# Optimization experiments

Hardware: AMD Instinct MI355X
Metric: run time of the kernel (lower is better)

The kernel has to match this reference:

```python
import jax, jax.numpy as jnp
import numpy as np

N_NODES = 100000
N_EDGES = 1600000
IN_F, HID_F, OUT_F = 128, 128, 128


def setup_inputs() -> dict:
    key = jax.random.key(0)
    k1, k2, k3, k4, k5, k6 = jax.random.split(key, 6)
    x = jax.random.normal(k1, (N_NODES, IN_F), dtype=jnp.float32)
    edge_index = jax.random.randint(k2, (2, N_EDGES), 0, N_NODES, dtype=jnp.int32)
    # nn.Linear params (PyTorch layout: W [out, in], y = x @ W.T + b)
    s1 = 1.0 / np.sqrt(IN_F)
    W1 = jax.random.uniform(k3, (HID_F, IN_F), minval=-s1, maxval=s1, dtype=jnp.float32)
    b1 = jax.random.uniform(k4, (HID_F,), minval=-s1, maxval=s1, dtype=jnp.float32)
    s2 = 1.0 / np.sqrt(HID_F)
    W2 = jax.random.uniform(k5, (OUT_F, HID_F), minval=-s2, maxval=s2, dtype=jnp.float32)
    b2 = jax.random.uniform(k6, (OUT_F,), minval=-s2, maxval=s2, dtype=jnp.float32)
    return {"x": x, "edge_index": edge_index, "W1": W1, "b1": b1, "W2": W2, "b2": b2}


def _spmm_mean(h, row, col, deg_inv):
    # (adj @ h)[i] = sum_{edges e: row[e]==i} h[col[e]], then scale by deg_inv[i]
    agg = jax.ops.segment_sum(h[col], row, num_segments=N_NODES)
    return agg * deg_inv[:, None]


def reference(x, edge_index, W1, b1, W2, b2):
    row, col = edge_index[0], edge_index[1]
    # degree = row-sum of adjacency (duplicates in COO are summed, matching torch)
    deg = jax.ops.segment_sum(jnp.ones((N_EDGES,), dtype=x.dtype), row, num_segments=N_NODES)
    deg_inv = jnp.where(deg > 0, 1.0 / deg, 0.0)
    # dropout in eval mode = identity
    h = x @ W1.T + b1
    h = _spmm_mean(h, row, col, deg_inv)
    h = jax.nn.elu(h)
    h = h @ W2.T + b2
    h = _spmm_mean(h, row, col, deg_inv)
    return h
```

## Files before the change

### kernel.cpp

```cpp
#include <hip/hip_runtime.h>
#include <math.h>

#define N_NODES 100000
#define N_EDGES 1600000
#define F 128
#define NBUCK 196
#define EPB 1024
#define CAP 9216

typedef _Float16 f16x2 __attribute__((ext_vector_type(2)));
typedef _Float16 f16x8 __attribute__((ext_vector_type(8)));
typedef __fp16 fp16x2 __attribute__((ext_vector_type(2)));
typedef float f32x2 __attribute__((ext_vector_type(2)));
typedef float f32x4 __attribute__((ext_vector_type(4)));

__device__ inline uint pkrtz(float a, float b) {
    union { fp16x2 h; uint u; } c;
    c.h = __builtin_amdgcn_cvt_pkrtz(a, b);
    return c.u;
}
__device__ inline f16x2 as2(uint u) {
    union { uint u; f16x2 h; } c; c.u = u; return c.h;
}

__device__ inline int wave_incl_scan(int v, int lane) {
#pragma unroll
    for (int off = 1; off < 64; off <<= 1) {
        int t = __shfl_up(v, off);
        if (lane >= off) v += t;
    }
    return v;
}


__global__ __launch_bounds__(256) void bucketize_kernel(const int* __restrict__ row,
                                                        const int* __restrict__ col,
                                                        int* __restrict__ bucket_cursor,
                                                        int* __restrict__ pairs) {
    __shared__ int stage[EPB];
    __shared__ unsigned char bid[EPB];
    __shared__ int lcnt[NBUCK], lcur[NBUCK], loff[NBUCK], gbase[NBUCK];
    __shared__ int wsum[4];
    const int tid = threadIdx.x;
    const int lane = tid & 63;
    const int wid = tid >> 6;
    const int base = blockIdx.x * EPB;
    const int cnt = min(N_EDGES - base, EPB);

    for (int i = tid; i < NBUCK; i += 256) { lcnt[i] = 0; lcur[i] = 0; }
    __syncthreads();
    for (int i = 0; i < EPB / 256; ++i) {
        int e = base + i * 256 + tid;
        if (e < N_EDGES) atomicAdd(&lcnt[row[e] >> 9], 1);
    }
    __syncthreads();
    {
        int v = (tid < NBUCK) ? lcnt[tid] : 0;
        int inc = wave_incl_scan(v, lane);
        if (lane == 63) wsum[wid] = inc;
        __syncthreads();
        if (tid == 0) {
            int a = 0;
#pragma unroll
            for (int i = 0; i < 4; ++i) { int t = wsum[i]; wsum[i] = a; a += t; }
        }
        __syncthreads();
        if (tid < NBUCK) loff[tid] = inc - v + wsum[wid];
    }
    if (tid < NBUCK) {
        int c = lcnt[tid];
        gbase[tid] = c ? atomicAdd(&bucket_cursor[tid], c) : 0;
    }
    __syncthreads();
    for (int i = 0; i < EPB / 256; ++i) {
        int e = base + i * 256 + tid;
        if (e < N_EDGES) {
            int r = row[e], c = col[e];
            int b = r >> 9;
            int rk = atomicAdd(&lcur[b], 1);
            int q = loff[b] + rk;
            stage[q] = ((r & 511) << 17) | c;
            bid[q] = (unsigned char)b;
        }
    }
    __syncthreads();
    for (int q = tid; q < cnt; q += 256) {
        int b = bid[q];
        int t = gbase[b] + (q - loff[b]);
        if (t < CAP) pairs[b * CAP + t] = stage[q];
    }
}

__global__ __launch_bounds__(1024) void csr_finalize_kernel(const int* __restrict__ pairs,
                                                            const int* __restrict__ bucket_cursor,
                                                            int* __restrict__ csr_col,
                                                            int2* __restrict__ rs,
                                                            float* __restrict__ deg_inv) {
    __shared__ int rcnt[512], rcnt2[512], roff[512];
    __shared__ int colstage[CAP];
    __shared__ int wsum[8];
    const int tid = threadIdx.x;
    const int lane = tid & 63;
    const int wid = tid >> 6;
    const int b = blockIdx.x;
    const int cnt = min(bucket_cursor[b], CAP);
    const int base = b * CAP;
    const int* reg = &pairs[base];

    if (tid < 512) { rcnt[tid] = 0; rcnt2[tid] = 0; }
    __syncthreads();
    for (int q = tid; q < cnt; q += 1024) atomicAdd(&rcnt[reg[q] >> 17], 1);
    __syncthreads();
    int d = 0, inc = 0;
    if (tid < 512) {
        d = rcnt[tid];
        inc = wave_incl_scan(d, lane);
        if (lane == 63) wsum[wid] = inc;
    }
    __syncthreads();
    if (tid == 0) {
        int a = 0;
#pragma unroll
        for (int i = 0; i < 8; ++i) { int t = wsum[i]; wsum[i] = a; a += t; }
    }
    __syncthreads();
    if (tid < 512) {
        const int excl = inc - d + wsum[wid];
        roff[tid] = excl;
        const int grow = (b << 9) + tid;
        if (grow < N_NODES) {
            rs[grow] = make_int2(base + excl, d);
            deg_inv[grow] = d ? 1.0f / (float)d : 0.0f;
        }
    }
    __syncthreads();
    for (int q = tid; q < cnt; q += 1024) {
        int v = reg[q];
        int lr = v >> 17;
        int rk = atomicAdd(&rcnt2[lr], 1);
        colstage[roff[lr] + rk] = v & 0x1FFFF;
    }
    __syncthreads();
    for (int q = tid; q < cnt; q += 1024) csr_col[base + q] = colstage[q];
}


__global__ __launch_bounds__(256) void convert_w_kernel(const float* __restrict__ W1,
                                                        const float* __restrict__ W2,
                                                        uint* __restrict__ W1h,
                                                        uint* __restrict__ W2h) {
    int i = blockIdx.x * 256 + threadIdx.x;
    if (i < F * F / 2) {
        float2 a = *(const float2*)&W1[i * 2];
        float2 b = *(const float2*)&W2[i * 2];
        W1h[i] = pkrtz(a.x, a.y);
        W2h[i] = pkrtz(b.x, b.y);
    }
}

__global__ __launch_bounds__(256) void convert_x_kernel(const float* __restrict__ X,
                                                        uint* __restrict__ Xh) {
    int i = blockIdx.x * 256 + threadIdx.x;
    if (i < N_NODES * F / 8) {
        float4 a = *(const float4*)&X[(size_t)i * 8];
        float4 b = *(const float4*)&X[(size_t)i * 8 + 4];
        uint4 o = {pkrtz(a.x, a.y), pkrtz(a.z, a.w), pkrtz(b.x, b.y), pkrtz(b.z, b.w)};
        *(uint4*)&Xh[(size_t)i * 4] = o;
    }
}


template <bool ELU, bool OUT_F32>
__global__ __launch_bounds__(64, 8) void fused_agg_gemm_kernel(
        const ushort* __restrict__ H,
        const int2* __restrict__ rs,
        const int* __restrict__ csr_col,
        const float* __restrict__ deg_inv,
        const ushort* __restrict__ Wh,
        const float* __restrict__ bias,
        void* __restrict__ out) {
    __shared__ __align__(16) ushort xs[16 * 136];

    const int tid = threadIdx.x;
    const int m0 = blockIdx.x << 4;
    const int qw = tid >> 4;
    const int fo = (tid & 15) << 3;

    for (int rr = 0; rr < 4; ++rr) {
        const int rowi = qw * 4 + rr;
        const int node = m0 + rowi;
        f32x2 a[4];
#pragma unroll
        for (int i = 0; i < 4; ++i) a[i] = (f32x2){0.f, 0.f};
        const int2 sd = rs[node];
        int p = sd.x;
        const int e = sd.x + sd.y;
        const float di = deg_inv[node];
        while (p + 7 < e) {
            int cc[8];
#pragma unroll
            for (int k = 0; k < 8; ++k) cc[k] = __builtin_nontemporal_load(&csr_col[p + k]);
            uint4 vv[8];
#pragma unroll
            for (int k = 0; k < 8; ++k) vv[k] = *(const uint4*)&H[(size_t)cc[k] * F + fo];
#pragma unroll
            for (int k = 0; k < 8; k += 4) {
                f16x2 h0 = (as2(vv[k].x) + as2(vv[k + 1].x)) + (as2(vv[k + 2].x) + as2(vv[k + 3].x));
                f16x2 h1 = (as2(vv[k].y) + as2(vv[k + 1].y)) + (as2(vv[k + 2].y) + as2(vv[k + 3].y));
                f16x2 h2 = (as2(vv[k].z) + as2(vv[k + 1].z)) + (as2(vv[k + 2].z) + as2(vv[k + 3].z));
                f16x2 h3 = (as2(vv[k].w) + as2(vv[k + 1].w)) + (as2(vv[k + 2].w) + as2(vv[k + 3].w));
                a[0] += (f32x2){(float)h0.x, (float)h0.y};
                a[1] += (f32x2){(float)h1.x, (float)h1.y};
                a[2] += (f32x2){(float)h2.x, (float)h2.y};
                a[3] += (f32x2){(float)h3.x, (float)h3.y};
            }
            p += 8;
        }
        if (p + 3 < e) {
            int c0 = csr_col[p], c1 = csr_col[p + 1], c2 = csr_col[p + 2], c3 = csr_col[p + 3];
            uint4 v0 = *(const uint4*)&H[(size_t)c0 * F + fo];
            uint4 v1 = *(const uint4*)&H[(size_t)c1 * F + fo];
            uint4 v2 = *(const uint4*)&H[(size_t)c2 * F + fo];
            uint4 v3 = *(const uint4*)&H[(size_t)c3 * F + fo];
            f16x2 h0 = (as2(v0.x) + as2(v1.x)) + (as2(v2.x) + as2(v3.x));
            f16x2 h1 = (as2(v0.y) + as2(v1.y)) + (as2(v2.y) + as2(v3.y));
            f16x2 h2 = (as2(v0.z) + as2(v1.z)) + (as2(v2.z) + as2(v3.z));
            f16x2 h3 = (as2(v0.w) + as2(v1.w)) + (as2(v2.w) + as2(v3.w));
            a[0] += (f32x2){(float)h0.x, (float)h0.y};
            a[1] += (f32x2){(float)h1.x, (float)h1.y};
            a[2] += (f32x2){(float)h2.x, (float)h2.y};
            a[3] += (f32x2){(float)h3.x, (float)h3.y};
            p += 4;
        }
        if (p + 1 < e) {
            int c0 = csr_col[p], c1 = csr_col[p + 1];
            uint4 v0 = *(const uint4*)&H[(size_t)c0 * F + fo];
            uint4 v1 = *(const uint4*)&H[(size_t)c1 * F + fo];
            f16x2 h0 = as2(v0.x) + as2(v1.x);
            f16x2 h1 = as2(v0.y) + as2(v1.y);
            f16x2 h2 = as2(v0.z) + as2(v1.z);
            f16x2 h3 = as2(v0.w) + as2(v1.w);
            a[0] += (f32x2){(float)h0.x, (float)h0.y};
            a[1] += (f32x2){(float)h1.x, (float)h1.y};
            a[2] += (f32x2){(float)h2.x, (float)h2.y};
            a[3] += (f32x2){(float)h3.x, (float)h3.y};
            p += 2;
        }
        if (p < e) {
            int c = csr_col[p];
            uint4 v = *(const uint4*)&H[(size_t)c * F + fo];
            f16x2 h0 = as2(v.x), h1 = as2(v.y), h2 = as2(v.z), h3 = as2(v.w);
            a[0] += (f32x2){(float)h0.x, (float)h0.y};
            a[1] += (f32x2){(float)h1.x, (float)h1.y};
            a[2] += (f32x2){(float)h2.x, (float)h2.y};
            a[3] += (f32x2){(float)h3.x, (float)h3.y};
        }
        uint4 o = {pkrtz(a[0].x * di, a[0].y * di), pkrtz(a[1].x * di, a[1].y * di),
                   pkrtz(a[2].x * di, a[2].y * di), pkrtz(a[3].x * di, a[3].y * di)};
        *(uint4*)&xs[rowi * 136 + fo] = o;
    }

    const int q = tid >> 4;
    const int t = tid & 15;

    f16x8 xfr[4];
#pragma unroll
    for (int kk = 0; kk < 4; ++kk)
        xfr[kk] = *(const f16x8*)&xs[t * 136 + kk * 32 + q * 8];

    f32x4 acc[8];
#pragma unroll
    for (int j = 0; j < 8; ++j) acc[j] = (f32x4){0.f, 0.f, 0.f, 0.f};

#pragma unroll
    for (int j = 0; j < 8; ++j) {
        const ushort* wrow = &Wh[(j * 16 + t) * F + q * 8];
#pragma unroll
        for (int kk = 0; kk < 4; ++kk) {
            f16x8 wfr = *(const f16x8*)&wrow[kk * 32];
            acc[j] = __builtin_amdgcn_mfma_f32_16x16x32_f16(wfr, xfr[kk], acc[j], 0, 0, 0);
        }
    }

    const int node = m0 + t;
    const float dv = deg_inv[node];
    const float mk = (dv > 0.f) ? 1.f : 0.f;

#pragma unroll
    for (int j = 0; j < 8; ++j) {
        f32x4 bb = *(const f32x4*)&bias[j * 16 + q * 4];
        f32x4 v = acc[j] + bb * mk;
        if (ELU) {
#pragma unroll
            for (int r = 0; r < 4; ++r) v[r] = (v[r] > 0.f) ? v[r] : expm1f(v[r]);
        }
        if (OUT_F32) {
            float* of = &((float*)out)[(size_t)node * F + j * 16 + q * 4];
            __builtin_nontemporal_store(v, (f32x4*)of);
        } else {
            uint2 o = {pkrtz(v[0], v[1]), pkrtz(v[2], v[3])};
            *(uint2*)&((ushort*)out)[(size_t)node * F + j * 16 + q * 4] = o;
        }
    }
}


extern "C" void kernel_launch(void* const* d_in, const int* in_sizes, int n_in,
                              void* d_out, int out_size, void* d_ws, size_t ws_size,
                              hipStream_t stream) {
    const float* x  = (const float*)d_in[0];
    const int*   ei = (const int*)d_in[1];
    const float* W1 = (const float*)d_in[2];
    const float* b1 = (const float*)d_in[3];
    const float* W2 = (const float*)d_in[4];
    const float* b2 = (const float*)d_in[5];
    float* out = (float*)d_out;

    const int* row = ei;
    const int* col = ei + N_EDGES;

    ushort* bufA = (ushort*)d_ws;
    ushort* bufB = bufA + (size_t)N_NODES * F;
    int* csr_col = (int*)(bufB + (size_t)N_NODES * F);
    int2* rs = (int2*)(csr_col + NBUCK * CAP);
    float* deg_inv = (float*)(rs + N_NODES + 4);
    int* bucket_cursor = (int*)(deg_inv + N_NODES);
    uint* W1h = (uint*)(bucket_cursor + 256);
    uint* W2h = W1h + F * F / 2;
    int* pairs = (int*)bufA;

    (void)hipMemsetAsync(bucket_cursor, 0, NBUCK * sizeof(int), stream);
    bucketize_kernel<<<(N_EDGES + EPB - 1) / EPB, 256, 0, stream>>>(row, col, bucket_cursor, pairs);
    csr_finalize_kernel<<<NBUCK, 1024, 0, stream>>>(pairs, bucket_cursor, csr_col, rs, deg_inv);

    convert_w_kernel<<<32, 256, 0, stream>>>(W1, W2, W1h, W2h);
    convert_x_kernel<<<N_NODES * F / 8 / 256, 256, 0, stream>>>(x, (uint*)bufB);

    const int fb = N_NODES / 16;
    fused_agg_gemm_kernel<true, false><<<fb, 64, 0, stream>>>(
        (const ushort*)bufB, rs, csr_col, deg_inv, (const ushort*)W1h, b1, bufA);
    fused_agg_gemm_kernel<false, true><<<fb, 64, 0, stream>>>(
        bufA, rs, csr_col, deg_inv, (const ushort*)W2h, b2, out);
}
```

Measured before the change: 336.7 us.

## Replace bucketed CSR build with degree-count, scan, atomic scatter; use 128-thread agg blocks

The two-pass bucket-then-sort CSR construction becomes three simple kernels. The first counts degrees with global atomics, the second computes per-bucket row offsets and cursors, and the third scatters columns through per-row atomic cursors. This removes the staging pass through the pairs buffer and the large shared-memory sort, at the cost of many contended global atomics and a nondeterministic column order within each row. The fused aggregation+GEMM kernel also switches to two waves per block with 32 rows per block, halving the block count.

```diff
diff --git a/kernel.cpp b/kernel.cpp
--- a/kernel.cpp
+++ b/kernel.cpp
@@ -5,7 +5,6 @@
 #define N_EDGES 1600000
 #define F 128
 #define NBUCK 196
-#define EPB 1024
 #define CAP 9216
 
 typedef _Float16 f16x2 __attribute__((ext_vector_type(2)));
@@ -33,90 +32,26 @@
 }
 
 
-__global__ __launch_bounds__(256) void bucketize_kernel(const int* __restrict__ row,
-                                                        const int* __restrict__ col,
-                                                        int* __restrict__ bucket_cursor,
-                                                        int* __restrict__ pairs) {
-    __shared__ int stage[EPB];
-    __shared__ unsigned char bid[EPB];
-    __shared__ int lcnt[NBUCK], lcur[NBUCK], loff[NBUCK], gbase[NBUCK];
-    __shared__ int wsum[4];
-    const int tid = threadIdx.x;
-    const int lane = tid & 63;
-    const int wid = tid >> 6;
-    const int base = blockIdx.x * EPB;
-    const int cnt = min(N_EDGES - base, EPB);
-
-    for (int i = tid; i < NBUCK; i += 256) { lcnt[i] = 0; lcur[i] = 0; }
-    __syncthreads();
-    for (int i = 0; i < EPB / 256; ++i) {
-        int e = base + i * 256 + tid;
-        if (e < N_EDGES) atomicAdd(&lcnt[row[e] >> 9], 1);
-    }
-    __syncthreads();
-    {
-        int v = (tid < NBUCK) ? lcnt[tid] : 0;
-        int inc = wave_incl_scan(v, lane);
-        if (lane == 63) wsum[wid] = inc;
-        __syncthreads();
-        if (tid == 0) {
-            int a = 0;
-#pragma unroll
-            for (int i = 0; i < 4; ++i) { int t = wsum[i]; wsum[i] = a; a += t; }
-        }
-        __syncthreads();
-        if (tid < NBUCK) loff[tid] = inc - v + wsum[wid];
-    }
-    if (tid < NBUCK) {
-        int c = lcnt[tid];
-        gbase[tid] = c ? atomicAdd(&bucket_cursor[tid], c) : 0;
-    }
-    __syncthreads();
-    for (int i = 0; i < EPB / 256; ++i) {
-        int e = base + i * 256 + tid;
-        if (e < N_EDGES) {
-            int r = row[e], c = col[e];
-            int b = r >> 9;
-            int rk = atomicAdd(&lcur[b], 1);
-            int q = loff[b] + rk;
-            stage[q] = ((r & 511) << 17) | c;
-            bid[q] = (unsigned char)b;
-        }
-    }
-    __syncthreads();
-    for (int q = tid; q < cnt; q += 256) {
-        int b = bid[q];
-        int t = gbase[b] + (q - loff[b]);
-        if (t < CAP) pairs[b * CAP + t] = stage[q];
-    }
-}
-
-__global__ __launch_bounds__(1024) void csr_finalize_kernel(const int* __restrict__ pairs,
-                                                            const int* __restrict__ bucket_cursor,
-                                                            int* __restrict__ csr_col,
-                                                            int2* __restrict__ rs,
-                                                            float* __restrict__ deg_inv) {
-    __shared__ int rcnt[512], rcnt2[512], roff[512];
-    __shared__ int colstage[CAP];
+__global__ __launch_bounds__(256) void deg_kernel(const int* __restrict__ row,
+                                                  int* __restrict__ deg) {
+    int e = blockIdx.x * 256 + threadIdx.x;
+    if (e < N_EDGES) atomicAdd(&deg[row[e]], 1);
+}
+
+__global__ __launch_bounds__(512) void rs_kernel(const int* __restrict__ deg,
+                                                 int2* __restrict__ rs,
+                                                 float* __restrict__ deg_inv,
+                                                 int* __restrict__ cursor) {
     __shared__ int wsum[8];
     const int tid = threadIdx.x;
     const int lane = tid & 63;
     const int wid = tid >> 6;
     const int b = blockIdx.x;
-    const int cnt = min(bucket_cursor[b], CAP);
+    const int grow = (b << 9) + tid;
     const int base = b * CAP;
-    const int* reg = &pairs[base];
-
-    if (tid < 512) { rcnt[tid] = 0; rcnt2[tid] = 0; }
-    __syncthreads();
-    for (int q = tid; q < cnt; q += 1024) atomicAdd(&rcnt[reg[q] >> 17], 1);
-    __syncthreads();
-    int d = 0, inc = 0;
-    if (tid < 512) {
-        d = rcnt[tid];
-        inc = wave_incl_scan(d, lane);
-        if (lane == 63) wsum[wid] = inc;
-    }
+    int d = (grow < N_NODES) ? deg[grow] : 0;
+    int inc = wave_incl_scan(d, lane);
+    if (lane == 63) wsum[wid] = inc;
     __syncthreads();
     if (tid == 0) {
         int a = 0;
@@ -124,24 +59,24 @@
         for (int i = 0; i < 8; ++i) { int t = wsum[i]; wsum[i] = a; a += t; }
     }
     __syncthreads();
-    if (tid < 512) {
-        const int excl = inc - d + wsum[wid];
-        roff[tid] = excl;
-        const int grow = (b << 9) + tid;
-        if (grow < N_NODES) {
-            rs[grow] = make_int2(base + excl, d);
-            deg_inv[grow] = d ? 1.0f / (float)d : 0.0f;
-        }
-    }
-    __syncthreads();
-    for (int q = tid; q < cnt; q += 1024) {
-        int v = reg[q];
-        int lr = v >> 17;
-        int rk = atomicAdd(&rcnt2[lr], 1);
-        colstage[roff[lr] + rk] = v & 0x1FFFF;
-    }
-    __syncthreads();
-    for (int q = tid; q < cnt; q += 1024) csr_col[base + q] = colstage[q];
+    const int excl = inc - d + wsum[wid];
+    if (grow < N_NODES) {
+        rs[grow] = make_int2(base + excl, d);
+        deg_inv[grow] = d ? 1.0f / (float)d : 0.0f;
+        cursor[grow] = base + excl;
+    }
+}
+
+__global__ __launch_bounds__(256) void scatter_kernel(const int* __restrict__ row,
+                                                      const int* __restrict__ col,
+                                                      int* __restrict__ cursor,
+                                                      int* __restrict__ csr_col) {
+    int e = blockIdx.x * 256 + threadIdx.x;
+    if (e < N_EDGES) {
+        int r = row[e], c = col[e];
+        int pos = atomicAdd(&cursor[r], 1);
+        if (pos < ((r >> 9) + 1) * CAP) csr_col[pos] = c;
+    }
 }
 
 
@@ -171,7 +106,7 @@
 
 
 template <bool ELU, bool OUT_F32>
-__global__ __launch_bounds__(64, 8) void fused_agg_gemm_kernel(
+__global__ __launch_bounds__(128, 8) void fused_agg_gemm_kernel(
         const ushort* __restrict__ H,
         const int2* __restrict__ rs,
         const int* __restrict__ csr_col,
@@ -179,12 +114,15 @@
         const ushort* __restrict__ Wh,
         const float* __restrict__ bias,
         void* __restrict__ out) {
-    __shared__ __align__(16) ushort xs[16 * 136];
+    __shared__ __align__(16) ushort xs[32 * 136];
 
     const int tid = threadIdx.x;
-    const int m0 = blockIdx.x << 4;
-    const int qw = tid >> 4;
-    const int fo = (tid & 15) << 3;
+    const int wv = tid >> 6;
+    const int lane = tid & 63;
+    const int m0 = (blockIdx.x << 5) + (wv << 4);
+    const int qw = lane >> 4;
+    const int fo = (lane & 15) << 3;
+    ushort* xw = &xs[(wv << 4) * 136];
 
     for (int rr = 0; rr < 4; ++rr) {
         const int rowi = qw * 4 + rr;
@@ -257,16 +195,16 @@
         }
         uint4 o = {pkrtz(a[0].x * di, a[0].y * di), pkrtz(a[1].x * di, a[1].y * di),
                    pkrtz(a[2].x * di, a[2].y * di), pkrtz(a[3].x * di, a[3].y * di)};
-        *(uint4*)&xs[rowi * 136 + fo] = o;
-    }
-
-    const int q = tid >> 4;
-    const int t = tid & 15;
+        *(uint4*)&xw[rowi * 136 + fo] = o;
+    }
+
+    const int q = lane >> 4;
+    const int t = lane & 15;
 
     f16x8 xfr[4];
 #pragma unroll
     for (int kk = 0; kk < 4; ++kk)
-        xfr[kk] = *(const f16x8*)&xs[t * 136 + kk * 32 + q * 8];
+        xfr[kk] = *(const f16x8*)&xw[t * 136 + kk * 32 + q * 8];
 
     f32x4 acc[8];
 #pragma unroll
@@ -324,21 +262,22 @@
     int* csr_col = (int*)(bufB + (size_t)N_NODES * F);
     int2* rs = (int2*)(csr_col + NBUCK * CAP);
     float* deg_inv = (float*)(rs + N_NODES + 4);
-    int* bucket_cursor = (int*)(deg_inv + N_NODES);
-    uint* W1h = (uint*)(bucket_cursor + 256);
+    uint* W1h = (uint*)(deg_inv + N_NODES);
     uint* W2h = W1h + F * F / 2;
-    int* pairs = (int*)bufA;
-
-    (void)hipMemsetAsync(bucket_cursor, 0, NBUCK * sizeof(int), stream);
-    bucketize_kernel<<<(N_EDGES + EPB - 1) / EPB, 256, 0, stream>>>(row, col, bucket_cursor, pairs);
-    csr_finalize_kernel<<<NBUCK, 1024, 0, stream>>>(pairs, bucket_cursor, csr_col, rs, deg_inv);
+    int* cursor = (int*)bufA;
+    int* deg = cursor + N_NODES;
+
+    (void)hipMemsetAsync(deg, 0, N_NODES * sizeof(int), stream);
+    deg_kernel<<<N_EDGES / 256, 256, 0, stream>>>(row, deg);
+    rs_kernel<<<NBUCK, 512, 0, stream>>>(deg, rs, deg_inv, cursor);
+    scatter_kernel<<<N_EDGES / 256, 256, 0, stream>>>(row, col, cursor, csr_col);
 
     convert_w_kernel<<<32, 256, 0, stream>>>(W1, W2, W1h, W2h);
     convert_x_kernel<<<N_NODES * F / 8 / 256, 256, 0, stream>>>(x, (uint*)bufB);
 
-    const int fb = N_NODES / 16;
-    fused_agg_gemm_kernel<true, false><<<fb, 64, 0, stream>>>(
+    const int fb = N_NODES / 32;
+    fused_agg_gemm_kernel<true, false><<<fb, 128, 0, stream>>>(
         (const ushort*)bufB, rs, csr_col, deg_inv, (const ushort*)W1h, b1, bufA);
-    fused_agg_gemm_kernel<false, true><<<fb, 64, 0, stream>>>(
+    fused_agg_gemm_kernel<false, true><<<fb, 128, 0, stream>>>(
         bufA, rs, csr_col, deg_inv, (const ushort*)W2h, b2, out);
 }
```

Result: slower. 466.8 us (+38.7%).
